# Optimization experiments

Measured on AMD Instinct MI355X. Metric: run time of the kernel, lower is better.

Reference implementation:

```python
import jax, jax.numpy as jnp
import numpy as np

B = 32768
INPUT_DIM = 128
MAX_DIM = 1024          # max_dynamic_reservoir_dim (pre-allocated)
ACTIVE = 512            # current_reservoir_size (runtime-active prefix)
LEAK = 0.2              # initial leak_rate
THRESH = 0.5            # initial spike_threshold


def setup_inputs() -> dict:
    key = jax.random.key(0)
    k = jax.random.split(key, 5)
    inputs = jax.random.normal(k[0], (B, INPUT_DIM), dtype=jnp.float32)
    prev_state = jax.random.normal(k[1], (B, MAX_DIM), dtype=jnp.float32)
    # Weights initialized like tf RandomNormal(stddev=0.1), pre-allocated to max dim
    W_res = 0.1 * jax.random.normal(k[2], (MAX_DIM, MAX_DIM), dtype=jnp.float32)
    W_in = 0.1 * jax.random.normal(k[3], (MAX_DIM, INPUT_DIM), dtype=jnp.float32)
    W_gate = 0.1 * jax.random.normal(k[4], (3 * MAX_DIM, INPUT_DIM), dtype=jnp.float32)
    # Trainable per-neuron params, initialized to inverse-sigmoid / inverse-softplus of initial values
    leak_rate_param = jnp.full((MAX_DIM,), np.log(LEAK / (1.0 - LEAK)), dtype=jnp.float32)
    spike_threshold_param = jnp.full((MAX_DIM,), np.log(np.expm1(THRESH)), dtype=jnp.float32)
    return {
        'inputs': inputs,
        'prev_state': prev_state,
        'W_res': W_res,
        'W_in': W_in,
        'W_gate': W_gate,
        'leak_rate_param': leak_rate_param,
        'spike_threshold_param': spike_threshold_param,
        'active_size': ACTIVE,
    }


def reference(inputs, prev_state, W_res, W_in, W_gate, leak_rate_param,
              spike_threshold_param, active_size):
    A = active_size
    max_dim = prev_state.shape[1]
    prev = prev_state[:, :A]                                   # [B, A]
    leak = jax.nn.sigmoid(leak_rate_param[:A])                 # [A]
    thr = jax.nn.softplus(spike_threshold_param[:A])           # [A]
    input_part = inputs @ W_in[:A, :].T                        # [B, A]
    reservoir_part = prev @ W_res[:A, :A]                      # [B, A]
    gates = jax.nn.sigmoid(inputs @ W_gate[:3 * A, :].T)       # [B, 3A]
    i_gate, f_gate, o_gate = jnp.split(gates, 3, axis=-1)
    state = (1.0 - leak) * (f_gate * prev) + leak * jnp.tanh(i_gate * (input_part + reservoir_part))
    state = o_gate * state
    # Threshold-triggered spiking reset: subtract threshold where state exceeds it
    state = jnp.where(state > thr, state - thr, state)
    # Pad active state back to the full pre-allocated reservoir width
    return jnp.pad(state, ((0, 0), (0, max_dim - A)))
```

## Files before the change

kernel.cpp:

```cpp
#include <hip/hip_runtime.h>
#include <cmath>

#define NB   32768
#define DIN  128
#define DMAX 1024
#define A    512

typedef _Float16 half8 __attribute__((ext_vector_type(8)));
typedef float f32x4 __attribute__((ext_vector_type(4)));

#define WS_RES_H 0
#define WS_RES_L 262144
#define WS_PAN   524288

#define SWZB(b) ((b) ^ ((((b) >> 6) & 7) << 4))
__device__ __forceinline__ unsigned swzh(unsigned h) { return h ^ (((h >> 5) & 7u) << 3); }

__device__ __forceinline__ float fsigm(float x) { return 1.0f / (1.0f + __expf(-x)); }
__device__ __forceinline__ float ftanh(float x) {
    float e = __expf(-2.0f * fabsf(x));
    float t = (1.0f - e) / (1.0f + e);
    return (x < 0.0f) ? -t : t;
}

__device__ __forceinline__ void gl16(const _Float16* src, _Float16* dst) {
    __builtin_amdgcn_global_load_lds(
        (const __attribute__((address_space(1))) unsigned int*)src,
        (__attribute__((address_space(3))) unsigned int*)dst, 16, 0, 0);
}

__global__ __launch_bounds__(256) void prep_w(
    const float* __restrict__ Wres, const float* __restrict__ Win,
    const float* __restrict__ Wg, _Float16* __restrict__ ws)
{
    int tid = blockIdx.x * 256 + threadIdx.x;
    float v[32];
    size_t dH, dL;
    int j = tid & 127;
    if (tid < 8192) {
        int c = tid >> 7;
        int jbb = c >> 4, kc = c & 15;
        int col = jbb * 128 + j;
#pragma unroll
        for (int i = 0; i < 32; ++i)
            v[i] = Wres[(size_t)(kc * 32 + i) * DMAX + col];
        dH = WS_RES_H + (size_t)c * 4096;
        dL = WS_RES_L + (size_t)c * 4096;
    } else {
        int r = tid - 8192;
        int c = r >> 7;
        int p = c >> 4, cc = c & 15;
        int jbb = cc >> 2, kc = cc & 3;
        int row = jbb * 128 + j;
        const float* s = (p == 0) ? (Win + (size_t)row * DIN + kc * 32)
                                  : (Wg + (size_t)((p - 1) * 512 + row) * DIN + kc * 32);
#pragma unroll
        for (int i = 0; i < 32; ++i) v[i] = s[i];
        dH = WS_PAN + (size_t)p * 131072 + (size_t)(jbb * 4 + kc) * 4096;
        dL = dH + 65536;
    }
#pragma unroll
    for (int g = 0; g < 4; ++g) {
        half8 hh, ll;
#pragma unroll
        for (int i = 0; i < 8; ++i) {
            float x = v[g * 8 + i];
            _Float16 h = (_Float16)x;
            hh[i] = h;
            ll[i] = (_Float16)(x - (float)h);
        }
        unsigned ho = swzh((unsigned)(j * 32 + g * 8));
        *(half8*)(ws + dH + ho) = hh;
        *(half8*)(ws + dL + ho) = ll;
    }
}

__global__ __launch_bounds__(256, 2) void gser3(
    const float* __restrict__ X,
    const float* __restrict__ P,
    const _Float16* __restrict__ ws,
    const float* __restrict__ lrp, const float* __restrict__ stp,
    float* __restrict__ out)
{
    __shared__ _Float16 lds[2][16384] __attribute__((aligned(16)));

    const int t    = threadIdx.x;
    const int lane = t & 63;
    const int w    = t >> 6;
    const int wm   = w & 1, wn = w >> 1;
    const int quad = lane >> 4, l16 = lane & 15;

    const int id = blockIdx.x;
    const int x8 = id & 7;
    const int s8 = id >> 3;
    const int jb = s8 & 3;
    const int g  = (s8 >> 2) * 8 + x8;
    const int m0 = g * 128;
    const int j0 = jb * 128;

    const float* Pblk = P + (size_t)m0 * DMAX;
    const float* Xblk = X + (size_t)m0 * DIN;

    int aOff[4], bOff[4];
#pragma unroll
    for (int ms = 0; ms < 4; ++ms) {
        int b = (wm * 64 + ms * 16 + l16) * 64 + quad * 16;
        aOff[ms] = SWZB(b);
    }
#pragma unroll
    for (int js = 0; js < 4; ++js) {
        int b = (wn * 64 + js * 16 + l16) * 64 + quad * 16;
        bOff[js] = SWZB(b);
    }

    const int sm = t >> 1;
    const int sk = (t & 1) * 16;

    auto stageB = [&](int buf, int s) {
        const _Float16 *chH, *chL;
        if (s < 16) {
            chH = ws + WS_RES_H + (size_t)(jb * 16 + s) * 4096;
            chL = ws + WS_RES_L + (size_t)(jb * 16 + s) * 4096;
        } else {
            int p = (s - 16) >> 2, kc = s & 3;
            chH = ws + WS_PAN + (size_t)p * 131072 + (size_t)(jb * 4 + kc) * 4096;
            chL = chH + 65536;
        }
        _Float16* l = &lds[buf][0];
        gl16(chH + w * 1024 + lane * 8,       l + 8192  + w * 1024);
        gl16(chH + w * 1024 + 512 + lane * 8, l + 8192  + w * 1024 + 512);
        gl16(chL + w * 1024 + lane * 8,       l + 12288 + w * 1024);
        gl16(chL + w * 1024 + 512 + lane * 8, l + 12288 + w * 1024 + 512);
    };

    auto writeA = [&](int buf, float4 r0, float4 r1, float4 r2, float4 r3) {
        float fv[16] = {r0.x,r0.y,r0.z,r0.w, r1.x,r1.y,r1.z,r1.w,
                        r2.x,r2.y,r2.z,r2.w, r3.x,r3.y,r3.z,r3.w};
        half8 h0, h1, l0, l1;
#pragma unroll
        for (int i = 0; i < 8; ++i) {
            _Float16 h = (_Float16)fv[i];
            h0[i] = h; l0[i] = (_Float16)(fv[i] - (float)h);
        }
#pragma unroll
        for (int i = 0; i < 8; ++i) {
            _Float16 h = (_Float16)fv[8 + i];
            h1[i] = h; l1[i] = (_Float16)(fv[8 + i] - (float)h);
        }
        char* base = (char*)&lds[buf][0];
        int a0 = SWZB(sm * 64 + sk * 2);
        int a1 = SWZB(sm * 64 + sk * 2 + 16);
        *(half8*)(base + a0) = h0;
        *(half8*)(base + a1) = h1;
        *(half8*)(base + 8192 + a0) = l0;
        *(half8*)(base + 8192 + a1) = l1;
    };

    auto mmac = [&](int buf, f32x4 (&C)[4][4]) {
        const char* base = (const char*)&lds[buf][0];
        half8 fah[4], fal[4];
#pragma unroll
        for (int ms = 0; ms < 4; ++ms) {
            fah[ms] = *(const half8*)(base + aOff[ms]);
            fal[ms] = *(const half8*)(base + 8192 + aOff[ms]);
        }
#pragma unroll
        for (int js = 0; js < 4; ++js) {
            half8 fbh = *(const half8*)(base + 16384 + bOff[js]);
            half8 fbl = *(const half8*)(base + 24576 + bOff[js]);
#pragma unroll
            for (int ms = 0; ms < 4; ++ms) {
                C[ms][js] = __builtin_amdgcn_mfma_f32_16x16x32_f16(fah[ms], fbh, C[ms][js], 0, 0, 0);
                C[ms][js] = __builtin_amdgcn_mfma_f32_16x16x32_f16(fah[ms], fbl, C[ms][js], 0, 0, 0);
                C[ms][js] = __builtin_amdgcn_mfma_f32_16x16x32_f16(fal[ms], fbh, C[ms][js], 0, 0, 0);
            }
        }
    };

    auto krnstep = [&](int s, f32x4 (&acc)[4][4], bool last) {
        const int bcur = s & 1, bnxt = bcur ^ 1;
        float4 r0, r1, r2, r3;
        if (!last) {
            const int sn = s + 1;
            const float* srcA = (sn < 16)
                ? (Pblk + (size_t)sm * DMAX + sn * 32 + sk)
                : (Xblk + (size_t)sm * DIN + (sn & 3) * 32 + sk);
            r0 = *(const float4*)(srcA);
            r1 = *(const float4*)(srcA + 4);
            r2 = *(const float4*)(srcA + 8);
            r3 = *(const float4*)(srcA + 12);
            stageB(bnxt, sn);
        }
        mmac(bcur, acc);
        if (!last) writeA(bnxt, r0, r1, r2, r3);
        __syncthreads();
    };

    f32x4 accS[4][4], accG[4][4];
#pragma unroll
    for (int i = 0; i < 4; ++i)
#pragma unroll
        for (int j = 0; j < 4; ++j)
            accS[i][j] = (f32x4){0.f, 0.f, 0.f, 0.f};

    {
        const float* srcA = Pblk + (size_t)sm * DMAX + sk;
        float4 r0 = *(const float4*)(srcA);
        float4 r1 = *(const float4*)(srcA + 4);
        float4 r2 = *(const float4*)(srcA + 8);
        float4 r3 = *(const float4*)(srcA + 12);
        stageB(0, 0);
        writeA(0, r0, r1, r2, r3);
        __syncthreads();
    }

    for (int s = 0; s < 20; ++s) krnstep(s, accS, false);

#pragma unroll
    for (int i = 0; i < 4; ++i)
#pragma unroll
        for (int j = 0; j < 4; ++j)
            accG[i][j] = (f32x4){0.f, 0.f, 0.f, 0.f};
    for (int s = 20; s < 24; ++s) krnstep(s, accG, false);
#pragma unroll
    for (int ms = 0; ms < 4; ++ms)
#pragma unroll
        for (int js = 0; js < 4; ++js)
#pragma unroll
            for (int r = 0; r < 4; ++r)
                accS[ms][js][r] = ftanh(fsigm(accG[ms][js][r]) * accS[ms][js][r]);

#pragma unroll
    for (int i = 0; i < 4; ++i)
#pragma unroll
        for (int j = 0; j < 4; ++j)
            accG[i][j] = (f32x4){0.f, 0.f, 0.f, 0.f};
    for (int s = 24; s < 28; ++s) krnstep(s, accG, false);
    {
        float lk[4];
#pragma unroll
        for (int js = 0; js < 4; ++js)
            lk[js] = fsigm(lrp[j0 + wn * 64 + js * 16 + l16]);
#pragma unroll
        for (int ms = 0; ms < 4; ++ms)
#pragma unroll
            for (int r = 0; r < 4; ++r) {
                int row = m0 + wm * 64 + ms * 16 + quad * 4 + r;
#pragma unroll
                for (int js = 0; js < 4; ++js) {
                    int col = j0 + wn * 64 + js * 16 + l16;
                    float pv = P[(size_t)row * DMAX + col];
                    float fg = fsigm(accG[ms][js][r]);
                    accS[ms][js][r] = (1.0f - lk[js]) * (fg * pv) + lk[js] * accS[ms][js][r];
                }
            }
    }

#pragma unroll
    for (int i = 0; i < 4; ++i)
#pragma unroll
        for (int j = 0; j < 4; ++j)
            accG[i][j] = (f32x4){0.f, 0.f, 0.f, 0.f};
    for (int s = 28; s < 31; ++s) krnstep(s, accG, false);
    krnstep(31, accG, true);
    {
        float thr[4];
#pragma unroll
        for (int js = 0; js < 4; ++js)
            thr[js] = log1pf(__expf(stp[j0 + wn * 64 + js * 16 + l16]));
#pragma unroll
        for (int ms = 0; ms < 4; ++ms)
#pragma unroll
            for (int r = 0; r < 4; ++r) {
                int row = m0 + wm * 64 + ms * 16 + quad * 4 + r;
#pragma unroll
                for (int js = 0; js < 4; ++js) {
                    int col = j0 + wn * 64 + js * 16 + l16;
                    float st = fsigm(accG[ms][js][r]) * accS[ms][js][r];
                    st = (st > thr[js]) ? (st - thr[js]) : st;
                    out[(size_t)row * DMAX + col] = st;
                }
            }
    }

#pragma unroll
    for (int i = 0; i < 16; ++i) {
        int s  = t + i * 256;
        int rr = s >> 5, c4 = s & 31;
        *(float4*)(out + (size_t)(m0 + rr) * DMAX + A + jb * 128 + c4 * 4) =
            (float4){0.f, 0.f, 0.f, 0.f};
    }
}

extern "C" void kernel_launch(void* const* d_in, const int* in_sizes, int n_in,
                              void* d_out, int out_size, void* d_ws, size_t ws_size,
                              hipStream_t stream) {
    const float* X    = (const float*)d_in[0];
    const float* P    = (const float*)d_in[1];
    const float* Wres = (const float*)d_in[2];
    const float* Win  = (const float*)d_in[3];
    const float* Wg   = (const float*)d_in[4];
    const float* lrp  = (const float*)d_in[5];
    const float* stp  = (const float*)d_in[6];
    float* out = (float*)d_out;
    _Float16* ws = (_Float16*)d_ws;

    hipLaunchKernelGGL(prep_w, dim3(64), dim3(256), 0, stream,
                       Wres, Win, Wg, ws);
    hipLaunchKernelGGL(gser3, dim3(1024), dim3(256), 0, stream,
                       X, P, ws, lrp, stp, out);
}
```

Before: 498.5 us.

## Load MFMA fragments directly from global memory and drop LDS staging

Removes the LDS double buffer and barriers entirely. Each wave now loads its A operand (fp32 prev-state or input rows) and its pre-split fp16 hi/lo B fragments straight from global memory into registers, and the weight workspace is written unswizzled to match. This is meant to remove LDS round-trips and __syncthreads costs. In exchange, each A row is fetched redundantly by the two waves sharing it (and B by the wn pairs), so global and L2 traffic goes up, register pressure rises, and load latency is only hidden by issuing the next step's loads before the MFMAs.

After: 524.3 us. +5.2%, slower.

```diff
diff --git a/kernel.cpp b/kernel.cpp
--- a/kernel.cpp
+++ b/kernel.cpp
@@ -12,21 +12,12 @@
 #define WS_RES_H 0
 #define WS_RES_L 262144
 #define WS_PAN   524288
-
-#define SWZB(b) ((b) ^ ((((b) >> 6) & 7) << 4))
-__device__ __forceinline__ unsigned swzh(unsigned h) { return h ^ (((h >> 5) & 7u) << 3); }
 
 __device__ __forceinline__ float fsigm(float x) { return 1.0f / (1.0f + __expf(-x)); }
 __device__ __forceinline__ float ftanh(float x) {
     float e = __expf(-2.0f * fabsf(x));
     float t = (1.0f - e) / (1.0f + e);
     return (x < 0.0f) ? -t : t;
-}
-
-__device__ __forceinline__ void gl16(const _Float16* src, _Float16* dst) {
-    __builtin_amdgcn_global_load_lds(
-        (const __attribute__((address_space(1))) unsigned int*)src,
-        (__attribute__((address_space(3))) unsigned int*)dst, 16, 0, 0);
 }
 
 __global__ __launch_bounds__(256) void prep_w(
@@ -60,30 +51,28 @@
         dL = dH + 65536;
     }
 #pragma unroll
-    for (int g = 0; g < 4; ++g) {
+    for (int gq = 0; gq < 4; ++gq) {
         half8 hh, ll;
 #pragma unroll
         for (int i = 0; i < 8; ++i) {
-            float x = v[g * 8 + i];
+            float x = v[gq * 8 + i];
             _Float16 h = (_Float16)x;
             hh[i] = h;
             ll[i] = (_Float16)(x - (float)h);
         }
-        unsigned ho = swzh((unsigned)(j * 32 + g * 8));
+        unsigned ho = (unsigned)(j * 32 + gq * 8);
         *(half8*)(ws + dH + ho) = hh;
         *(half8*)(ws + dL + ho) = ll;
     }
 }
 
-__global__ __launch_bounds__(256, 2) void gser3(
+__global__ __launch_bounds__(256, 2) void gser4(
     const float* __restrict__ X,
     const float* __restrict__ P,
     const _Float16* __restrict__ ws,
     const float* __restrict__ lrp, const float* __restrict__ stp,
     float* __restrict__ out)
 {
-    __shared__ _Float16 lds[2][16384] __attribute__((aligned(16)));
-
     const int t    = threadIdx.x;
     const int lane = t & 63;
     const int w    = t >> 6;
@@ -101,22 +90,44 @@
     const float* Pblk = P + (size_t)m0 * DMAX;
     const float* Xblk = X + (size_t)m0 * DIN;
 
-    int aOff[4], bOff[4];
-#pragma unroll
-    for (int ms = 0; ms < 4; ++ms) {
-        int b = (wm * 64 + ms * 16 + l16) * 64 + quad * 16;
-        aOff[ms] = SWZB(b);
-    }
-#pragma unroll
-    for (int js = 0; js < 4; ++js) {
-        int b = (wn * 64 + js * 16 + l16) * 64 + quad * 16;
-        bOff[js] = SWZB(b);
-    }
-
-    const int sm = t >> 1;
-    const int sk = (t & 1) * 16;
-
-    auto stageB = [&](int buf, int s) {
+    half8 fah[4], fal[4];
+    half8 fbh[4], fbl[4];
+    f32x4 ra[4][2];
+
+    auto loadRaw = [&](int s) {
+        const float* base;
+        int lda;
+        if (s < 16) { base = Pblk + s * 32;       lda = DMAX; }
+        else        { base = Xblk + (s & 3) * 32; lda = DIN;  }
+#pragma unroll
+        for (int ms = 0; ms < 4; ++ms) {
+            const float* p = base + (size_t)(wm * 64 + ms * 16 + l16) * lda + quad * 8;
+            ra[ms][0] = *(const f32x4*)p;
+            ra[ms][1] = *(const f32x4*)(p + 4);
+        }
+    };
+
+    auto convA = [&]() {
+#pragma unroll
+        for (int ms = 0; ms < 4; ++ms) {
+            half8 hh, ll;
+#pragma unroll
+            for (int i = 0; i < 4; ++i) {
+                float v0 = ra[ms][0][i];
+                float v1 = ra[ms][1][i];
+                _Float16 h0 = (_Float16)v0;
+                _Float16 h1 = (_Float16)v1;
+                hh[i]     = h0;
+                hh[4 + i] = h1;
+                ll[i]     = (_Float16)(v0 - (float)h0);
+                ll[4 + i] = (_Float16)(v1 - (float)h1);
+            }
+            fah[ms] = hh;
+            fal[ms] = ll;
+        }
+    };
+
+    auto loadB = [&](int s) {
         const _Float16 *chH, *chL;
         if (s < 16) {
             chH = ws + WS_RES_H + (size_t)(jb * 16 + s) * 4096;
@@ -126,74 +137,30 @@
             chH = ws + WS_PAN + (size_t)p * 131072 + (size_t)(jb * 4 + kc) * 4096;
             chL = chH + 65536;
         }
-        _Float16* l = &lds[buf][0];
-        gl16(chH + w * 1024 + lane * 8,       l + 8192  + w * 1024);
-        gl16(chH + w * 1024 + 512 + lane * 8, l + 8192  + w * 1024 + 512);
-        gl16(chL + w * 1024 + lane * 8,       l + 12288 + w * 1024);
-        gl16(chL + w * 1024 + 512 + lane * 8, l + 12288 + w * 1024 + 512);
-    };
-
-    auto writeA = [&](int buf, float4 r0, float4 r1, float4 r2, float4 r3) {
-        float fv[16] = {r0.x,r0.y,r0.z,r0.w, r1.x,r1.y,r1.z,r1.w,
-                        r2.x,r2.y,r2.z,r2.w, r3.x,r3.y,r3.z,r3.w};
-        half8 h0, h1, l0, l1;
-#pragma unroll
-        for (int i = 0; i < 8; ++i) {
-            _Float16 h = (_Float16)fv[i];
-            h0[i] = h; l0[i] = (_Float16)(fv[i] - (float)h);
-        }
-#pragma unroll
-        for (int i = 0; i < 8; ++i) {
-            _Float16 h = (_Float16)fv[8 + i];
-            h1[i] = h; l1[i] = (_Float16)(fv[8 + i] - (float)h);
-        }
-        char* base = (char*)&lds[buf][0];
-        int a0 = SWZB(sm * 64 + sk * 2);
-        int a1 = SWZB(sm * 64 + sk * 2 + 16);
-        *(half8*)(base + a0) = h0;
-        *(half8*)(base + a1) = h1;
-        *(half8*)(base + 8192 + a0) = l0;
-        *(half8*)(base + 8192 + a1) = l1;
-    };
-
-    auto mmac = [&](int buf, f32x4 (&C)[4][4]) {
-        const char* base = (const char*)&lds[buf][0];
-        half8 fah[4], fal[4];
-#pragma unroll
-        for (int ms = 0; ms < 4; ++ms) {
-            fah[ms] = *(const half8*)(base + aOff[ms]);
-            fal[ms] = *(const half8*)(base + 8192 + aOff[ms]);
-        }
 #pragma unroll
         for (int js = 0; js < 4; ++js) {
-            half8 fbh = *(const half8*)(base + 16384 + bOff[js]);
-            half8 fbl = *(const half8*)(base + 24576 + bOff[js]);
+            int off = (wn * 64 + js * 16 + l16) * 32 + quad * 8;
+            fbh[js] = *(const half8*)(chH + off);
+            fbl[js] = *(const half8*)(chL + off);
+        }
+    };
+
+    auto mmac = [&](f32x4 (&C)[4][4]) {
+#pragma unroll
+        for (int js = 0; js < 4; ++js)
 #pragma unroll
             for (int ms = 0; ms < 4; ++ms) {
-                C[ms][js] = __builtin_amdgcn_mfma_f32_16x16x32_f16(fah[ms], fbh, C[ms][js], 0, 0, 0);
-                C[ms][js] = __builtin_amdgcn_mfma_f32_16x16x32_f16(fah[ms], fbl, C[ms][js], 0, 0, 0);
-                C[ms][js] = __builtin_amdgcn_mfma_f32_16x16x32_f16(fal[ms], fbh, C[ms][js], 0, 0, 0);
-            }
-        }
-    };
-
-    auto krnstep = [&](int s, f32x4 (&acc)[4][4], bool last) {
-        const int bcur = s & 1, bnxt = bcur ^ 1;
-        float4 r0, r1, r2, r3;
-        if (!last) {
-            const int sn = s + 1;
-            const float* srcA = (sn < 16)
-                ? (Pblk + (size_t)sm * DMAX + sn * 32 + sk)
-                : (Xblk + (size_t)sm * DIN + (sn & 3) * 32 + sk);
-            r0 = *(const float4*)(srcA);
-            r1 = *(const float4*)(srcA + 4);
-            r2 = *(const float4*)(srcA + 8);
-            r3 = *(const float4*)(srcA + 12);
-            stageB(bnxt, sn);
-        }
-        mmac(bcur, acc);
-        if (!last) writeA(bnxt, r0, r1, r2, r3);
-        __syncthreads();
+                C[ms][js] = __builtin_amdgcn_mfma_f32_16x16x32_f16(fah[ms], fbh[js], C[ms][js], 0, 0, 0);
+                C[ms][js] = __builtin_amdgcn_mfma_f32_16x16x32_f16(fah[ms], fbl[js], C[ms][js], 0, 0, 0);
+                C[ms][js] = __builtin_amdgcn_mfma_f32_16x16x32_f16(fal[ms], fbh[js], C[ms][js], 0, 0, 0);
+            }
+    };
+
+    auto step = [&](int s, f32x4 (&acc)[4][4], int snext) {
+        loadB(s);
+        if (snext >= 0) loadRaw(snext);
+        mmac(acc);
+        if (snext >= 0) convA();
     };
 
     f32x4 accS[4][4], accG[4][4];
@@ -203,25 +170,17 @@
         for (int j = 0; j < 4; ++j)
             accS[i][j] = (f32x4){0.f, 0.f, 0.f, 0.f};
 
-    {
-        const float* srcA = Pblk + (size_t)sm * DMAX + sk;
-        float4 r0 = *(const float4*)(srcA);
-        float4 r1 = *(const float4*)(srcA + 4);
-        float4 r2 = *(const float4*)(srcA + 8);
-        float4 r3 = *(const float4*)(srcA + 12);
-        stageB(0, 0);
-        writeA(0, r0, r1, r2, r3);
-        __syncthreads();
-    }
-
-    for (int s = 0; s < 20; ++s) krnstep(s, accS, false);
+    loadRaw(0);
+    convA();
+
+    for (int s = 0; s < 20; ++s) step(s, accS, s + 1);
 
 #pragma unroll
     for (int i = 0; i < 4; ++i)
 #pragma unroll
         for (int j = 0; j < 4; ++j)
             accG[i][j] = (f32x4){0.f, 0.f, 0.f, 0.f};
-    for (int s = 20; s < 24; ++s) krnstep(s, accG, false);
+    for (int s = 20; s < 24; ++s) step(s, accG, s + 1);
 #pragma unroll
     for (int ms = 0; ms < 4; ++ms)
 #pragma unroll
@@ -235,7 +194,7 @@
 #pragma unroll
         for (int j = 0; j < 4; ++j)
             accG[i][j] = (f32x4){0.f, 0.f, 0.f, 0.f};
-    for (int s = 24; s < 28; ++s) krnstep(s, accG, false);
+    for (int s = 24; s < 28; ++s) step(s, accG, s + 1);
     {
         float lk[4];
 #pragma unroll
@@ -261,8 +220,7 @@
 #pragma unroll
         for (int j = 0; j < 4; ++j)
             accG[i][j] = (f32x4){0.f, 0.f, 0.f, 0.f};
-    for (int s = 28; s < 31; ++s) krnstep(s, accG, false);
-    krnstep(31, accG, true);
+    for (int s = 28; s < 32; ++s) step(s, accG, (s < 31) ? s + 1 : -1);
     {
         float thr[4];
 #pragma unroll
@@ -307,6 +265,6 @@
 
     hipLaunchKernelGGL(prep_w, dim3(64), dim3(256), 0, stream,
                        Wres, Win, Wg, ws);
-    hipLaunchKernelGGL(gser3, dim3(1024), dim3(256), 0, stream,
+    hipLaunchKernelGGL(gser4, dim3(1024), dim3(256), 0, stream,
                        X, P, ws, lrp, stp, out);
 }
```
